# Optimization experiments

Hardware: AMD Instinct MI355X
Metric: run time of the kernel (lower is better)

Reference implementation:

```python
import jax, jax.numpy as jnp
import numpy as np

FEATURE_SIZE = 10 * 64 * 64  # 40960
HIDDEN1 = 512
HIDDEN2 = 256
BATCH = 4096


def setup_inputs() -> dict:
    key = jax.random.key(0)
    ks = jax.random.split(key, 8)
    # Sparse binary-ish features emulated as dense uniform (math is identical).
    white_features = jax.random.uniform(ks[0], (BATCH, FEATURE_SIZE), dtype=jnp.float32)
    black_features = jax.random.uniform(ks[1], (BATCH, FEATURE_SIZE), dtype=jnp.float32)
    s_ft = 1.0 / np.sqrt(FEATURE_SIZE)
    s_fc1 = 1.0 / np.sqrt(HIDDEN1 * 2)
    s_fc2 = 1.0 / np.sqrt(HIDDEN2)
    ft_w = jax.random.uniform(ks[2], (HIDDEN1, FEATURE_SIZE), minval=-s_ft, maxval=s_ft, dtype=jnp.float32)
    ft_b = jax.random.uniform(ks[3], (HIDDEN1,), minval=-s_ft, maxval=s_ft, dtype=jnp.float32)
    fc1_w = jax.random.uniform(ks[4], (HIDDEN2, HIDDEN1 * 2), minval=-s_fc1, maxval=s_fc1, dtype=jnp.float32)
    fc1_b = jax.random.uniform(ks[5], (HIDDEN2,), minval=-s_fc1, maxval=s_fc1, dtype=jnp.float32)
    fc2_w = jax.random.uniform(ks[6], (1, HIDDEN2), minval=-s_fc2, maxval=s_fc2, dtype=jnp.float32)
    fc2_b = jax.random.uniform(ks[7], (1,), minval=-s_fc2, maxval=s_fc2, dtype=jnp.float32)
    return dict(white_features=white_features, black_features=black_features,
                ft_w=ft_w, ft_b=ft_b, fc1_w=fc1_w, fc1_b=fc1_b, fc2_w=fc2_w, fc2_b=fc2_b)


def reference(white_features, black_features, ft_w, ft_b, fc1_w, fc1_b, fc2_w, fc2_b):
    # Feature transform per perspective, clamped to [0, 1]
    white_ft = jnp.clip(white_features @ ft_w.T + ft_b, 0.0, 1.0)  # [B, H1]
    black_ft = jnp.clip(black_features @ ft_w.T + ft_b, 0.0, 1.0)  # [B, H1]
    combined = jnp.concatenate([white_ft, black_ft], axis=1)       # [B, 2*H1]
    x = jax.nn.relu(combined @ fc1_w.T + fc1_b)                    # [B, H2]
    x = x @ fc2_w.T + fc2_b                                        # [B, 1]
    return x.squeeze(-1)
```

## Files before the change

kernel.cpp:

```cpp
#include <hip/hip_runtime.h>
#include <stdint.h>

#define BATCH 4096
#define FEAT  40960
#define H1    512
#define KS    4
#define KCHUNK (FEAT / KS)
#define NSTEPS (KCHUNK / 32)
#define NMACRO (KCHUNK / 128)
#define NTILES (FEAT / 32)
#define WTILE  32768

typedef float f32x4 __attribute__((ext_vector_type(4)));
typedef short s16x8 __attribute__((ext_vector_type(8)));
typedef unsigned int u32x2 __attribute__((ext_vector_type(2)));
typedef unsigned int u32x4 __attribute__((ext_vector_type(4)));

__device__ __forceinline__ unsigned bfpack2(float lo, float hi) {
  unsigned a = __float_as_uint(lo);
  unsigned b = __float_as_uint(hi);
  a += 0x7FFFu + ((a >> 16) & 1u);
  b += 0x7FFFu + ((b >> 16) & 1u);
  return (a >> 16) | (b & 0xFFFF0000u);
}

__device__ __forceinline__ unsigned cvtpk(float lo, float hi) {
  unsigned r;
  asm("v_cvt_pk_bf16_f32 %0, %1, %2" : "=v"(r) : "v"(lo), "v"(hi));
  return r;
}

__device__ __forceinline__ int lds_swz(int r, int cb) {
  return (r << 6) + (cb ^ (((r >> 1) & 3) << 4));
}

__device__ __forceinline__ void glds16(const void* g, void* l) {
  __builtin_amdgcn_global_load_lds(
      (const __attribute__((address_space(1))) unsigned*)g,
      (__attribute__((address_space(3))) unsigned*)l, 16, 0, 0);
}

#define SFENCE() __builtin_amdgcn_sched_barrier(0)

__global__ __launch_bounds__(512)
void wcvt_kernel(const float* __restrict__ ftw, char* __restrict__ wbf) {
  const int T = blockIdx.x;
  const int tid = threadIdx.x;
  const int c  = tid & 7;
  const int r0 = tid >> 3;
#pragma unroll
  for (int pass = 0; pass < 8; ++pass) {
    const int r = pass * 64 + r0;
    const float* src = ftw + (size_t)r * FEAT + T * 32 + c * 4;
    f32x4 v = *(const f32x4*)src;
    u32x2 o;
    o.x = bfpack2(v.x, v.y);
    o.y = bfpack2(v.z, v.w);
    const int nb = r >> 6, f = (r >> 4) & 3, lr = r & 15;
    const int l = (c >> 1) * 16 + lr;
    *(u32x2*)(wbf + (size_t)T * WTILE + ((nb * 4 + f) << 10) + l * 16 +
              (c & 1) * 8) = o;
  }
}

__global__ __launch_bounds__(512, 4)
void ft_gemm_kernel(const float* __restrict__ whiteF,
                    const float* __restrict__ blackF,
                    const char* __restrict__ wbf,
                    float* __restrict__ Ppart) {
  __shared__ char smem[65536];

  const int tid = threadIdx.x, bid = blockIdx.x;
  const int wgid = (bid & 7) * 64 + (bid >> 3);
  const int ks = wgid >> 7;
  const int p  = (wgid >> 6) & 1;
  const int mt = wgid & 63;

  const float* Ag =
      (p == 0 ? whiteF : blackF) + (size_t)(mt * 64) * FEAT + ks * KCHUNK;
  const char* Agc = (const char*)Ag;

  const int lane = tid & 63, wave = tid >> 6;
  const int lrow = lane & 15, lkq = lane >> 4;

  unsigned aoff[4];
  int adst[4];
  const int c31 = lane & 31;
#pragma unroll
  for (int j = 0; j < 4; ++j) {
    const int rr = wave * 8 + 2 * j + (lane >> 5);
    aoff[j] = (unsigned)rr * (FEAT * 4u) + (unsigned)((c31 ^ (rr & 7)) << 4);
    adst[j] = (wave * 8 + 2 * j) * 512;
  }

  int adA[4][2];
#pragma unroll
  for (int m = 0; m < 4; ++m)
#pragma unroll
    for (int i = 0; i < 2; ++i)
      adA[m][i] = (m * 16 + lrow) * 512 + ((((lkq << 1) | i) ^ (lrow & 7)) << 4);

  const char* wptr =
      wbf + (size_t)(ks * NSTEPS) * WTILE + (wave << 12) + lane * 16;

  f32x4 acc[4][4];
#pragma unroll
  for (int m = 0; m < 4; ++m)
#pragma unroll
    for (int n = 0; n < 4; ++n) acc[m][n] = (f32x4){0.f, 0.f, 0.f, 0.f};

  u32x4 wb[4];

#pragma unroll
  for (int j = 0; j < 4; ++j) glds16(Agc + aoff[j], smem + adst[j]);
  SFENCE();
#pragma unroll
  for (int n = 0; n < 4; ++n) wb[n] = *(const u32x4*)(wptr + (n << 10));
#pragma unroll
  for (int j = 0; j < 4; ++j) aoff[j] += 512;
  asm volatile("s_waitcnt vmcnt(4)" ::: "memory");
  SFENCE();
  __builtin_amdgcn_s_barrier();
  SFENCE();

#define MICRO(B, JM, T)                                                       \
  {                                                                           \
    s16x8 af[4];                                                              \
    _Pragma("unroll") for (int m = 0; m < 4; ++m) {                           \
      f32x4 lo = *(const f32x4*)(smem + adA[m][0] + (B) * 32768 + (JM) * 128);\
      f32x4 hi = *(const f32x4*)(smem + adA[m][1] + (B) * 32768 + (JM) * 128);\
      u32x4 cv;                                                               \
      cv.x = cvtpk(lo.x, lo.y); cv.y = cvtpk(lo.z, lo.w);                     \
      cv.z = cvtpk(hi.x, hi.y); cv.w = cvtpk(hi.z, hi.w);                     \
      af[m] = __builtin_bit_cast(s16x8, cv);                                  \
    }                                                                         \
    _Pragma("unroll") for (int n = 0; n < 4; ++n)                             \
      _Pragma("unroll") for (int m = 0; m < 4; ++m)                           \
          acc[m][n] = __builtin_amdgcn_mfma_f32_16x16x32_bf16(                \
              af[m], __builtin_bit_cast(s16x8, wb[n]), acc[m][n], 0, 0, 0);   \
    if ((JM) < 3) {            \
      const char* wsp = wptr + (size_t)(4 * (T) + (JM) + 1) * WTILE;          \
      _Pragma("unroll") for (int n = 0; n < 4; ++n)                           \
          wb[n] = *(const u32x4*)(wsp + (n << 10));                           \
      glds16(Agc + aoff[JM], smem + (((B) ^ 1) * 32768) + adst[JM]);          \
    } else {        \
      glds16(Agc + aoff[3], smem + (((B) ^ 1) * 32768) + adst[3]);            \
      SFENCE();                                                               \
      const char* wsp = wptr + (size_t)(4 * (T) + 4) * WTILE;                 \
      _Pragma("unroll") for (int n = 0; n < 4; ++n)                           \
          wb[n] = *(const u32x4*)(wsp + (n << 10));                           \
    }                                                                         \
  }

#define MACRO(B, T)                                                           \
  {                                                                           \
    MICRO(B, 0, T);                                                           \
    MICRO(B, 1, T);                                                           \
    MICRO(B, 2, T);                                                           \
    MICRO(B, 3, T);                                                           \
    asm volatile("s_waitcnt vmcnt(4)" ::: "memory");        \
    SFENCE();                                                                 \
    __builtin_amdgcn_s_barrier();                                             \
    SFENCE();                                                                 \
    const unsigned adv = ((T) + 2 < NMACRO) ? 512u : 0u;                      \
    _Pragma("unroll") for (int j = 0; j < 4; ++j) aoff[j] += adv;             \
  }

  for (int TT = 0; TT < NMACRO; TT += 2) {
    MACRO(0, TT);
    MACRO(1, TT + 1);
  }
#undef MACRO
#undef MICRO

  asm volatile("s_waitcnt vmcnt(0) lgkmcnt(0)" ::: "memory");
  SFENCE();

  float* Pp = Ppart + ((size_t)(ks * 2 + p) * BATCH + mt * 64) * H1;
  const int r0 = lkq * 4;
  const int c0 = wave * 64 + lrow;
#pragma unroll
  for (int m = 0; m < 4; ++m)
#pragma unroll
    for (int n = 0; n < 4; ++n) {
      float* dst = Pp + (size_t)(r0 + m * 16) * H1 + c0 + n * 16;
#pragma unroll
      for (int j = 0; j < 4; ++j) dst[(size_t)j * H1] = acc[m][n][j];
    }
}

__global__ __launch_bounds__(256)
void ft_reduce_kernel(const float* __restrict__ Ppart,
                      const float* __restrict__ ftb,
                      unsigned short* __restrict__ comb) {
  const size_t gid = (size_t)blockIdx.x * 256 + threadIdx.x;
  const int    pp  = (int)(gid / (BATCH * H1 / 4));
  const size_t rem = gid % (BATCH * H1 / 4);
  const int    row = (int)(rem / (H1 / 4));
  const int    n4  = (int)(rem % (H1 / 4)) * 4;

  f32x4 s = (f32x4){0.f, 0.f, 0.f, 0.f};
#pragma unroll
  for (int ks = 0; ks < KS; ++ks)
    s += *(const f32x4*)(Ppart + ((size_t)(ks * 2 + pp) * BATCH + row) * H1 + n4);
  const f32x4 bv = *(const f32x4*)(ftb + n4);
  s += bv;
  s.x = fminf(fmaxf(s.x, 0.f), 1.f);
  s.y = fminf(fmaxf(s.y, 0.f), 1.f);
  s.z = fminf(fmaxf(s.z, 0.f), 1.f);
  s.w = fminf(fmaxf(s.w, 0.f), 1.f);

  u32x2 o;
  o.x = bfpack2(s.x, s.y);
  o.y = bfpack2(s.z, s.w);
  *(u32x2*)(comb + (size_t)row * 1024 + pp * H1 + n4) = o;
}

__global__ __launch_bounds__(256)
void fc_kernel(const unsigned short* __restrict__ comb,
               const float* __restrict__ w1, const float* __restrict__ b1,
               const float* __restrict__ w2, const float* __restrict__ b2,
               float* __restrict__ out) {
  __shared__ char smem[40960];
  __shared__ float rowsum[64];

  const int tid = threadIdx.x;
  const int bm  = blockIdx.x;
  if (tid < 64) rowsum[tid] = 0.f;

  const int a_row = tid >> 2, a_kq = tid & 3;
  const unsigned short* aptr = comb + (size_t)(bm * 64 + a_row) * 1024 + a_kq * 8;
  const float* wptr = w1 + (size_t)a_row * 1024 + a_kq * 8;

  u32x4 raA;
  f32x4 rw0[4], rw1[4];
  auto issue = [&](int t) {
    raA = *(const u32x4*)(aptr + t * 32);
    const float* wp = wptr + t * 32;
#pragma unroll
    for (int s = 0; s < 4; ++s) {
      rw0[s] = *(const f32x4*)(wp + (size_t)s * 64 * 1024);
      rw1[s] = *(const f32x4*)(wp + (size_t)s * 64 * 1024 + 4);
    }
  };

  const int aoff_w = lds_swz(a_row, a_kq * 16);
  int woff_w[4];
#pragma unroll
  for (int s = 0; s < 4; ++s)
    woff_w[s] = 4096 + lds_swz(s * 64 + a_row, a_kq * 16);

  auto cvtwrite = [&](int b) {
    char* base = smem + b * 20480;
    *(u32x4*)(base + aoff_w) = raA;
#pragma unroll
    for (int s = 0; s < 4; ++s) {
      u32x4 wv;
      wv.x = bfpack2(rw0[s].x, rw0[s].y); wv.y = bfpack2(rw0[s].z, rw0[s].w);
      wv.z = bfpack2(rw1[s].x, rw1[s].y); wv.w = bfpack2(rw1[s].z, rw1[s].w);
      *(u32x4*)(base + woff_w[s]) = wv;
    }
  };

  const int lane = tid & 63, wn = tid >> 6;
  const int lrow = lane & 15, lkb = (lane >> 4) * 16;
  int a_off[4], b_off[4];
#pragma unroll
  for (int m = 0; m < 4; ++m) a_off[m] = lds_swz(m * 16 + lrow, lkb);
#pragma unroll
  for (int n = 0; n < 4; ++n) b_off[n] = 4096 + lds_swz(wn * 64 + n * 16 + lrow, lkb);

  f32x4 acc[4][4];
#pragma unroll
  for (int m = 0; m < 4; ++m)
#pragma unroll
    for (int n = 0; n < 4; ++n) acc[m][n] = (f32x4){0.f, 0.f, 0.f, 0.f};

  issue(0);
  for (int t = 0; t < 32; ++t) {
    const int b = t & 1;
    cvtwrite(b);
    if (t + 1 < 32) issue(t + 1);
    asm volatile("s_waitcnt lgkmcnt(0)" ::: "memory");
    __builtin_amdgcn_sched_barrier(0);
    __builtin_amdgcn_s_barrier();
    __builtin_amdgcn_sched_barrier(0);
    char* base = smem + b * 20480;
    s16x8 af[4];
#pragma unroll
    for (int m = 0; m < 4; ++m) af[m] = *(const s16x8*)(base + a_off[m]);
#pragma unroll
    for (int n = 0; n < 4; ++n) {
      s16x8 bfn = *(const s16x8*)(base + b_off[n]);
#pragma unroll
      for (int m = 0; m < 4; ++m)
        acc[m][n] = __builtin_amdgcn_mfma_f32_16x16x32_bf16(af[m], bfn, acc[m][n], 0, 0, 0);
    }
  }

  float b1v[4], w2v[4];
#pragma unroll
  for (int n = 0; n < 4; ++n) {
    const int col = wn * 64 + n * 16 + lrow;
    b1v[n] = b1[col];
    w2v[n] = w2[col];
  }
#pragma unroll
  for (int m = 0; m < 4; ++m)
#pragma unroll
    for (int j = 0; j < 4; ++j) {
      float v = 0.f;
#pragma unroll
      for (int n = 0; n < 4; ++n) {
        float x = acc[m][n][j] + b1v[n];
        x = fmaxf(x, 0.f);
        v += x * w2v[n];
      }
#pragma unroll
      for (int d = 1; d < 16; d <<= 1) v += __shfl_xor(v, d, 64);
      if ((lane & 15) == 0)
        atomicAdd(&rowsum[m * 16 + (lane >> 4) * 4 + j], v);
    }
  __syncthreads();
  if (tid < 64) {
    out[bm * 64 + tid] = rowsum[tid] + b2[0];
  }
}

extern "C" void kernel_launch(void* const* d_in, const int* in_sizes, int n_in,
                              void* d_out, int out_size, void* d_ws, size_t ws_size,
                              hipStream_t stream) {
  const float* whiteF = (const float*)d_in[0];
  const float* blackF = (const float*)d_in[1];
  const float* ftw    = (const float*)d_in[2];
  const float* ftb    = (const float*)d_in[3];
  const float* w1     = (const float*)d_in[4];
  const float* b1     = (const float*)d_in[5];
  const float* w2     = (const float*)d_in[6];
  const float* b2     = (const float*)d_in[7];

  char* wbf = (char*)d_ws;
  const size_t wbf_bytes   = (size_t)NTILES * WTILE;
  const size_t ppart_bytes = (size_t)KS * 2 * BATCH * H1 * sizeof(float);
  float* Ppart = (float*)((char*)d_ws + wbf_bytes);
  unsigned short* comb = (unsigned short*)((char*)d_ws + wbf_bytes + ppart_bytes);
  float* outp = (float*)d_out;

  hipLaunchKernelGGL(wcvt_kernel, dim3(NTILES), dim3(512), 0, stream, ftw, wbf);
  hipLaunchKernelGGL(ft_gemm_kernel, dim3(512), dim3(512), 0, stream,
                     whiteF, blackF, wbf, Ppart);
  hipLaunchKernelGGL(ft_reduce_kernel, dim3((2 * BATCH * H1 / 4) / 256), dim3(256),
                     0, stream, Ppart, ftb, comb);
  hipLaunchKernelGGL(fc_kernel, dim3(BATCH / 64), dim3(256), 0, stream,
                     comb, w1, b1, w2, b2, outp);
}
```

Measured before the change: 638.2 us.

## Halve split-K, double A slab size, and deepen weight register prefetch

Reduces split-K from 4 to 2, so 256 workgroups each process a larger K range. A slabs now hold 256 K columns (128 KB LDS double buffer), loaded in one batch mid-macro. Weight fragments are prefetched four micro-steps ahead in a 4-deep register ring instead of one. This cuts partial-sum traffic and barrier count, at the cost of halved grid size and occupancy, more registers, and a larger reduction buffer footprint mismatch (ft_reduce may still assume KS).

```diff
diff --git a/kernel.cpp b/kernel.cpp
--- a/kernel.cpp
+++ b/kernel.cpp
@@ -4,12 +4,13 @@
 #define BATCH 4096
 #define FEAT  40960
 #define H1    512
-#define KS    4
+#define KS    2
 #define KCHUNK (FEAT / KS)
-#define NSTEPS (KCHUNK / 32)
-#define NMACRO (KCHUNK / 128)
+#define NMACRO (KCHUNK / 256)
+#define NMICRO (KCHUNK / 32)
 #define NTILES (FEAT / 32)
 #define WTILE  32768
+#define SLAB   65536
 
 typedef float f32x4 __attribute__((ext_vector_type(4)));
 typedef short s16x8 __attribute__((ext_vector_type(8)));
@@ -63,15 +64,15 @@
   }
 }
 
-__global__ __launch_bounds__(512, 4)
+__global__ __launch_bounds__(512, 2)
 void ft_gemm_kernel(const float* __restrict__ whiteF,
                     const float* __restrict__ blackF,
                     const char* __restrict__ wbf,
                     float* __restrict__ Ppart) {
-  __shared__ char smem[65536];
+  __shared__ char smem[2 * SLAB];
 
   const int tid = threadIdx.x, bid = blockIdx.x;
-  const int wgid = (bid & 7) * 64 + (bid >> 3);
+  const int wgid = (bid & 7) * 32 + (bid >> 3);
   const int ks = wgid >> 7;
   const int p  = (wgid >> 6) & 1;
   const int mt = wgid & 63;
@@ -82,15 +83,15 @@
 
   const int lane = tid & 63, wave = tid >> 6;
   const int lrow = lane & 15, lkq = lane >> 4;
-
-  unsigned aoff[4];
-  int adst[4];
-  const int c31 = lane & 31;
-#pragma unroll
-  for (int j = 0; j < 4; ++j) {
-    const int rr = wave * 8 + 2 * j + (lane >> 5);
-    aoff[j] = (unsigned)rr * (FEAT * 4u) + (unsigned)((c31 ^ (rr & 7)) << 4);
-    adst[j] = (wave * 8 + 2 * j) * 512;
+  const int rx7 = lrow & 7;
+
+  const char* asrc[8];
+  int adst[8];
+#pragma unroll
+  for (int i = 0; i < 8; ++i) {
+    const int row = wave * 8 + i;
+    asrc[i] = Agc + (size_t)row * (FEAT * 4) + ((lane ^ i) << 4);
+    adst[i] = row * 1024;
   }
 
   int adA[4][2];
@@ -98,10 +99,10 @@
   for (int m = 0; m < 4; ++m)
 #pragma unroll
     for (int i = 0; i < 2; ++i)
-      adA[m][i] = (m * 16 + lrow) * 512 + ((((lkq << 1) | i) ^ (lrow & 7)) << 4);
-
-  const char* wptr =
-      wbf + (size_t)(ks * NSTEPS) * WTILE + (wave << 12) + lane * 16;
+      adA[m][i] = (m * 16 + lrow) * 1024 + ((((lkq << 1) | i) ^ rx7) << 4);
+
+  const char* wsrc =
+      wbf + (size_t)(ks * NMICRO) * WTILE + (wave << 12) + lane * 16;
 
   f32x4 acc[4][4];
 #pragma unroll
@@ -109,26 +110,29 @@
 #pragma unroll
     for (int n = 0; n < 4; ++n) acc[m][n] = (f32x4){0.f, 0.f, 0.f, 0.f};
 
-  u32x4 wb[4];
-
-#pragma unroll
-  for (int j = 0; j < 4; ++j) glds16(Agc + aoff[j], smem + adst[j]);
-  SFENCE();
-#pragma unroll
-  for (int n = 0; n < 4; ++n) wb[n] = *(const u32x4*)(wptr + (n << 10));
-#pragma unroll
-  for (int j = 0; j < 4; ++j) aoff[j] += 512;
-  asm volatile("s_waitcnt vmcnt(4)" ::: "memory");
+  u32x4 wb[4][4];
+
+#pragma unroll
+  for (int s = 0; s < 4; ++s) {
+    const char* wsp = wsrc + (size_t)s * WTILE;
+#pragma unroll
+    for (int n = 0; n < 4; ++n) wb[s][n] = *(const u32x4*)(wsp + (n << 10));
+  }
+  SFENCE();
+#pragma unroll
+  for (int i = 0; i < 8; ++i) glds16(asrc[i], smem + adst[i]);
+  SFENCE();
+  asm volatile("s_waitcnt vmcnt(0)" ::: "memory");
   SFENCE();
   __builtin_amdgcn_s_barrier();
   SFENCE();
 
-#define MICRO(B, JM, T)                                                       \
+#define MICRO(B, J, t)                                                        \
   {                                                                           \
     s16x8 af[4];                                                              \
     _Pragma("unroll") for (int m = 0; m < 4; ++m) {                           \
-      f32x4 lo = *(const f32x4*)(smem + adA[m][0] + (B) * 32768 + (JM) * 128);\
-      f32x4 hi = *(const f32x4*)(smem + adA[m][1] + (B) * 32768 + (JM) * 128);\
+      f32x4 lo = *(const f32x4*)(smem + (B) * SLAB + adA[m][0] + (J) * 128);  \
+      f32x4 hi = *(const f32x4*)(smem + (B) * SLAB + adA[m][1] + (J) * 128);  \
       u32x4 cv;                                                               \
       cv.x = cvtpk(lo.x, lo.y); cv.y = cvtpk(lo.z, lo.w);                     \
       cv.z = cvtpk(hi.x, hi.y); cv.w = cvtpk(hi.z, hi.w);                     \
@@ -137,38 +141,37 @@
     _Pragma("unroll") for (int n = 0; n < 4; ++n)                             \
       _Pragma("unroll") for (int m = 0; m < 4; ++m)                           \
           acc[m][n] = __builtin_amdgcn_mfma_f32_16x16x32_bf16(                \
-              af[m], __builtin_bit_cast(s16x8, wb[n]), acc[m][n], 0, 0, 0);   \
-    if ((JM) < 3) {            \
-      const char* wsp = wptr + (size_t)(4 * (T) + (JM) + 1) * WTILE;          \
+              af[m], __builtin_bit_cast(s16x8, wb[(J) & 3][n]),               \
+              acc[m][n], 0, 0, 0);                                            \
+    {                     \
+      int g = (t) * 8 + (J) + 4;                                              \
+      if (g >= NMICRO) g = NMICRO - 1;                                        \
+      const char* wsp = wsrc + (size_t)g * WTILE;                             \
       _Pragma("unroll") for (int n = 0; n < 4; ++n)                           \
-          wb[n] = *(const u32x4*)(wsp + (n << 10));                           \
-      glds16(Agc + aoff[JM], smem + (((B) ^ 1) * 32768) + adst[JM]);          \
-    } else {        \
-      glds16(Agc + aoff[3], smem + (((B) ^ 1) * 32768) + adst[3]);            \
-      SFENCE();                                                               \
-      const char* wsp = wptr + (size_t)(4 * (T) + 4) * WTILE;                 \
-      _Pragma("unroll") for (int n = 0; n < 4; ++n)                           \
-          wb[n] = *(const u32x4*)(wsp + (n << 10));                           \
+          wb[(J) & 3][n] = *(const u32x4*)(wsp + (n << 10));                  \
     }                                                                         \
   }
 
 #define MACRO(B, T)                                                           \
   {                                                                           \
-    MICRO(B, 0, T);                                                           \
-    MICRO(B, 1, T);                                                           \
-    MICRO(B, 2, T);                                                           \
-    MICRO(B, 3, T);                                                           \
-    asm volatile("s_waitcnt vmcnt(4)" ::: "memory");        \
+    MICRO(B, 0, T); MICRO(B, 1, T); MICRO(B, 2, T); MICRO(B, 3, T);           \
+    SFENCE();                                                                 \
+    if ((T) + 1 < NMACRO) {      \
+      _Pragma("unroll") for (int i = 0; i < 8; ++i)                           \
+          glds16(asrc[i] + (size_t)((T) + 1) * 1024,                          \
+                 smem + ((B) ^ 1) * SLAB + adst[i]);                          \
+    }                                                                         \
+    SFENCE();                                                                 \
+    MICRO(B, 4, T); MICRO(B, 5, T); MICRO(B, 6, T); MICRO(B, 7, T);           \
+    asm volatile("s_waitcnt vmcnt(16)" ::: "memory");           \
     SFENCE();                                                                 \
     __builtin_amdgcn_s_barrier();                                             \
     SFENCE();                                                                 \
-    const unsigned adv = ((T) + 2 < NMACRO) ? 512u : 0u;                      \
-    _Pragma("unroll") for (int j = 0; j < 4; ++j) aoff[j] += adv;             \
-  }
-
-  for (int TT = 0; TT < NMACRO; TT += 2) {
-    MACRO(0, TT);
-    MACRO(1, TT + 1);
+  }
+
+  for (int t = 0; t < NMACRO; t += 2) {
+    MACRO(0, t);
+    MACRO(1, t + 1);
   }
 #undef MACRO
 #undef MICRO
@@ -347,7 +350,7 @@
   float* outp = (float*)d_out;
 
   hipLaunchKernelGGL(wcvt_kernel, dim3(NTILES), dim3(512), 0, stream, ftw, wbf);
-  hipLaunchKernelGGL(ft_gemm_kernel, dim3(512), dim3(512), 0, stream,
+  hipLaunchKernelGGL(ft_gemm_kernel, dim3(256), dim3(512), 0, stream,
                      whiteF, blackF, wbf, Ppart);
   hipLaunchKernelGGL(ft_reduce_kernel, dim3((2 * BATCH * H1 / 4) / 256), dim3(256),
                      0, stream, Ppart, ftb, comb);
```

Result: faster. 570.1 us (-10.7%).
